# Kernel tuning notes

Measured on AMD Instinct MI355X. Metric: run time of the kernel, lower is better.

The kernel has to match this reference:

```python
import jax, jax.numpy as jnp
import numpy as np
import math

B, S, D = 2, 512, 768
N_HEADS, HEAD = 12, 64
ALPHA = 32.0


def setup_inputs() -> dict:
    key = jax.random.key(0)
    ks = jax.random.split(key, 12)
    w_scale = 1.0 / math.sqrt(D)
    return {
        "hidden_states": jax.random.normal(ks[0], (B, S, D), jnp.float32),
        "attention_mask": jnp.zeros((B, 1, 1, S), jnp.float32),
        "rel_pos": jax.random.normal(ks[1], (B, S, S, HEAD), jnp.float32),
        "rel_2d_pos": jax.random.normal(ks[2], (B, S, S, HEAD), jnp.float32),
        "rel_2d_angle": jax.random.normal(ks[3], (B, S, S, HEAD), jnp.float32),
        "Wq": jax.random.normal(ks[4], (D, D), jnp.float32) * w_scale,
        "bq": jnp.zeros((D,), jnp.float32),
        "Wk": jax.random.normal(ks[5], (D, D), jnp.float32) * w_scale,
        "bk": jnp.zeros((D,), jnp.float32),
        "Wv": jax.random.normal(ks[6], (D, D), jnp.float32) * w_scale,
        "bv": jnp.zeros((D,), jnp.float32),
    }


def _heads(x):
    # (B,S,D) -> (B,N,S,HEAD)
    b, s, _ = x.shape
    return x.reshape(b, s, N_HEADS, HEAD).transpose(0, 2, 1, 3)


def reference(hidden_states, attention_mask, rel_pos, rel_2d_pos, rel_2d_angle,
              Wq, bq, Wk, bk, Wv, bv):
    q = _heads(hidden_states @ Wq.T + bq)
    k = _heads(hidden_states @ Wk.T + bk)
    v = _heads(hidden_states @ Wv.T + bv)

    qs = q / math.sqrt(HEAD)  # scaled query, (B,N,S,HEAD)
    scores = jnp.einsum('bnsh,bnkh->bnsk', qs, k)
    scores = scores + jnp.einsum('bnsh,bskh->bnsk', qs, rel_pos)
    scores = scores + jnp.einsum('bnsh,bskh->bnsk', qs, rel_2d_pos)
    scores = scores + jnp.einsum('bnsh,bskh->bnsk', qs, rel_2d_angle)
    scores = scores + attention_mask

    # cogview (PB-Relax) softmax: subtract per-row max of scores/alpha, rescale
    scaled = scores / ALPHA
    m = jnp.max(scaled, axis=-1, keepdims=True)
    probs = jax.nn.softmax((scaled - m) * ALPHA, axis=-1)

    ctx = jnp.einsum('bnsk,bnkh->bsnh', probs, v)  # (B,S,N,HEAD)
    return ctx.reshape(ctx.shape[0], ctx.shape[1], N_HEADS * HEAD)
```

## Files before the change

### kernel.cpp

```cpp
#include <hip/hip_runtime.h>

typedef __attribute__((ext_vector_type(8))) short short8;
typedef __attribute__((ext_vector_type(4))) float f32x4;

#define B_ 2
#define S_ 512
#define D_ 768
#define NH 12
#define HD 64

__device__ inline short f2bf(float f) {
    union { float f; unsigned u; } v; v.f = f;
    unsigned r = v.u + 0x7fffu + ((v.u >> 16) & 1u);
    return (short)(r >> 16);
}

__device__ __forceinline__ f32x4 ntload4(const float* p) {
    return __builtin_nontemporal_load((const f32x4*)p);
}

__global__ __launch_bounds__(256) void qkv_gemm(
    const float* __restrict__ hidden,
    const float* __restrict__ Wq, const float* __restrict__ Wk, const float* __restrict__ Wv,
    const float* __restrict__ bq, const float* __restrict__ bk, const float* __restrict__ bv,
    short* __restrict__ qbf, short* __restrict__ kbf, short* __restrict__ vbf)
{
    __shared__ short hs[64 * 72];
    __shared__ short wt[64 * 72];

    const int mt = blockIdx.x, nt = blockIdx.y, mat = blockIdx.z;
    const int m0 = mt * 64, n0 = nt * 64;
    const float* W    = (mat == 0) ? Wq : ((mat == 1) ? Wk : Wv);
    const float* bias = (mat == 0) ? bq : ((mat == 1) ? bk : bv);

    const int tid = threadIdx.x;
    const int w = tid >> 6, l = tid & 63;
    const int sr = tid >> 2, sc = (tid & 3) * 16;

    f32x4 acc[4];
    #pragma unroll
    for (int i = 0; i < 4; ++i) acc[i] = (f32x4){0.f, 0.f, 0.f, 0.f};

    const int arow = (w * 16 + (l & 15)) * 72 + (l >> 4) * 8;

    for (int kt = 0; kt < 12; ++kt) {
        const int d0 = kt * 64;
        if (kt) __syncthreads();
        {
            const float4* sa = (const float4*)(hidden + (size_t)(m0 + sr) * D_ + d0 + sc);
            float4 x0 = sa[0], x1 = sa[1], x2 = sa[2], x3 = sa[3];
            short8 p0 = {f2bf(x0.x), f2bf(x0.y), f2bf(x0.z), f2bf(x0.w),
                         f2bf(x1.x), f2bf(x1.y), f2bf(x1.z), f2bf(x1.w)};
            short8 p1 = {f2bf(x2.x), f2bf(x2.y), f2bf(x2.z), f2bf(x2.w),
                         f2bf(x3.x), f2bf(x3.y), f2bf(x3.z), f2bf(x3.w)};
            *(short8*)&hs[sr * 72 + sc]     = p0;
            *(short8*)&hs[sr * 72 + sc + 8] = p1;
            const float4* sb = (const float4*)(W + (size_t)(n0 + sr) * D_ + d0 + sc);
            float4 y0 = sb[0], y1 = sb[1], y2 = sb[2], y3 = sb[3];
            short8 q0 = {f2bf(y0.x), f2bf(y0.y), f2bf(y0.z), f2bf(y0.w),
                         f2bf(y1.x), f2bf(y1.y), f2bf(y1.z), f2bf(y1.w)};
            short8 q1 = {f2bf(y2.x), f2bf(y2.y), f2bf(y2.z), f2bf(y2.w),
                         f2bf(y3.x), f2bf(y3.y), f2bf(y3.z), f2bf(y3.w)};
            *(short8*)&wt[sr * 72 + sc]     = q0;
            *(short8*)&wt[sr * 72 + sc + 8] = q1;
        }
        __syncthreads();
        short8 a0 = *(const short8*)&hs[arow];
        short8 a1 = *(const short8*)&hs[arow + 32];
        #pragma unroll
        for (int ct = 0; ct < 4; ++ct) {
            const int brow = (ct * 16 + (l & 15)) * 72 + (l >> 4) * 8;
            short8 b0 = *(const short8*)&wt[brow];
            short8 b1 = *(const short8*)&wt[brow + 32];
            acc[ct] = __builtin_amdgcn_mfma_f32_16x16x32_bf16(a0, b0, acc[ct], 0, 0, 0);
            acc[ct] = __builtin_amdgcn_mfma_f32_16x16x32_bf16(a1, b1, acc[ct], 0, 0, 0);
        }
    }

    if (mat == 2) {
        __syncthreads();
        #pragma unroll
        for (int ct = 0; ct < 4; ++ct) {
            #pragma unroll
            for (int rr = 0; rr < 4; ++rr) {
                const int m_l = w * 16 + (l >> 4) * 4 + rr;
                const int n_l = ct * 16 + (l & 15);
                hs[n_l * 68 + m_l] = f2bf(acc[ct][rr] + bias[n0 + n_l]);
            }
        }
        __syncthreads();
        const int b   = m0 >> 9;
        const int s0b = m0 & 511;
        #pragma unroll
        for (int j = 0; j < 2; ++j) {
            const int idx  = j * 256 + tid;
            const int h    = idx >> 3;
            const int sseg = (idx & 7) * 8;
            short8 vv = *(const short8*)&hs[h * 68 + sseg];
            *(short8*)(vbf + ((size_t)(b * NH + nt) * HD + h) * S_ + s0b + sseg) = vv;
        }
    } else {
        #pragma unroll
        for (int ct = 0; ct < 4; ++ct) {
            #pragma unroll
            for (int rr = 0; rr < 4; ++rr) {
                const int m_l = w * 16 + (l >> 4) * 4 + rr;
                const int n_l = ct * 16 + (l & 15);
                const int m = m0 + m_l;
                const int b = m >> 9, s = m & 511;
                float v = acc[ct][rr] + bias[n0 + n_l];
                const size_t dst = (((size_t)(b * NH + nt) * S_) + s) * HD + n_l;
                if (mat == 0) qbf[dst] = f2bf(v * 0.125f);
                else          kbf[dst] = f2bf(v);
            }
        }
    }
}

__global__ __launch_bounds__(256) void score_rel(
    const short* __restrict__ qbf,
    const float* __restrict__ rel1, const float* __restrict__ rel2, const float* __restrict__ rel3,
    float* __restrict__ relsc)
{
    const int kt = blockIdx.x;
    const int s  = blockIdx.y;
    const int b  = blockIdx.z;
    const int tid = threadIdx.x;
    const int w = tid >> 6, l = tid & 63;

    const int rowsel = l & 15;
    const int hc     = (l >> 4) * 8;

    const int kc = kt * 4 + w;
    const size_t rbase = ((size_t)(b * S_ + s)) * S_ * HD;
    const size_t ro = rbase + (size_t)(kc * 16 + rowsel) * HD + hc;

    f32x4 p0a = ntload4(rel1 + ro);
    f32x4 p0b = ntload4(rel1 + ro + 4);
    f32x4 q0a = ntload4(rel1 + ro + 32);
    f32x4 q0b = ntload4(rel1 + ro + 36);
    f32x4 p1a = ntload4(rel2 + ro);
    f32x4 p1b = ntload4(rel2 + ro + 4);
    f32x4 q1a = ntload4(rel2 + ro + 32);
    f32x4 q1b = ntload4(rel2 + ro + 36);
    f32x4 p2a = ntload4(rel3 + ro);
    f32x4 p2b = ntload4(rel3 + ro + 4);
    f32x4 q2a = ntload4(rel3 + ro + 32);
    f32x4 q2b = ntload4(rel3 + ro + 36);

    short8 a0 = {0, 0, 0, 0, 0, 0, 0, 0};
    short8 a1 = {0, 0, 0, 0, 0, 0, 0, 0};
    if (rowsel < NH) {
        const short* qp = qbf + (((size_t)(b * NH + rowsel) * S_) + s) * HD;
        a0 = *(const short8*)(qp + hc);
        a1 = *(const short8*)(qp + hc + 32);
    }

    short8 b0 = {
        f2bf(p0a.x + p1a.x + p2a.x), f2bf(p0a.y + p1a.y + p2a.y),
        f2bf(p0a.z + p1a.z + p2a.z), f2bf(p0a.w + p1a.w + p2a.w),
        f2bf(p0b.x + p1b.x + p2b.x), f2bf(p0b.y + p1b.y + p2b.y),
        f2bf(p0b.z + p1b.z + p2b.z), f2bf(p0b.w + p1b.w + p2b.w)};
    short8 b1 = {
        f2bf(q0a.x + q1a.x + q2a.x), f2bf(q0a.y + q1a.y + q2a.y),
        f2bf(q0a.z + q1a.z + q2a.z), f2bf(q0a.w + q1a.w + q2a.w),
        f2bf(q0b.x + q1b.x + q2b.x), f2bf(q0b.y + q1b.y + q2b.y),
        f2bf(q0b.z + q1b.z + q2b.z), f2bf(q0b.w + q1b.w + q2b.w)};

    f32x4 acc = (f32x4){0.f, 0.f, 0.f, 0.f};
    acc = __builtin_amdgcn_mfma_f32_16x16x32_bf16(a0, b0, acc, 0, 0, 0);
    acc = __builtin_amdgcn_mfma_f32_16x16x32_bf16(a1, b1, acc, 0, 0, 0);

    const int kg = kc * 16 + rowsel;
    #pragma unroll
    for (int rr = 0; rr < 4; ++rr) {
        const int n = (l >> 4) * 4 + rr;
        if (n < NH)
            relsc[(((size_t)(b * S_ + s)) * NH + n) * S_ + kg] = acc[rr];
    }
}

__global__ __launch_bounds__(256) void smqkpv(
    const short* __restrict__ qbf, const short* __restrict__ kbf,
    const float* __restrict__ relsc, const float* __restrict__ mask,
    const short* __restrict__ vbf, float* __restrict__ out)
{
    __shared__ float sc[16][520];
    __shared__ short pbf[16][520];

    const int st  = blockIdx.x;
    const int n   = blockIdx.y;
    const int b   = blockIdx.z;
    const int s0  = st * 16;
    const int tid = threadIdx.x;
    const int w = tid >> 6, l = tid & 63;

    const int arow = l & 15;
    const int g    = l >> 4;

    const short* qp = qbf + (((size_t)(b * NH + n) * S_) + s0 + arow) * HD + g * 8;
    short8 a0 = *(const short8*)(qp);
    short8 a1 = *(const short8*)(qp + 32);

    f32x4 acc[8];
    #pragma unroll
    for (int t = 0; t < 8; ++t) acc[t] = (f32x4){0.f, 0.f, 0.f, 0.f};

    #pragma unroll
    for (int t = 0; t < 8; ++t) {
        const int k0 = (w * 8 + t) * 16;
        const short* kp = kbf + (((size_t)(b * NH + n) * S_) + k0 + arow) * HD + g * 8;
        short8 b0 = *(const short8*)(kp);
        short8 b1 = *(const short8*)(kp + 32);
        acc[t] = __builtin_amdgcn_mfma_f32_16x16x32_bf16(a0, b0, acc[t], 0, 0, 0);
        acc[t] = __builtin_amdgcn_mfma_f32_16x16x32_bf16(a1, b1, acc[t], 0, 0, 0);
    }

    #pragma unroll
    for (int t = 0; t < 8; ++t) {
        const int k0 = (w * 8 + t) * 16;
        #pragma unroll
        for (int rr = 0; rr < 4; ++rr)
            sc[g * 4 + rr][k0 + arow] = acc[t][rr];
    }
    __syncthreads();

    #pragma unroll
    for (int j = 0; j < 8; ++j) {
        const int fidx = j * 256 + tid;
        const int row  = fidx >> 7;
        const int c4   = (fidx & 127) * 4;
        float4 r = *(const float4*)(relsc +
                    (((size_t)(b * S_ + s0 + row)) * NH + n) * S_ + c4);
        float4 mk = *(const float4*)(mask + b * S_ + c4);
        float4 cur = *(const float4*)&sc[row][c4];
        cur.x += r.x + mk.x; cur.y += r.y + mk.y;
        cur.z += r.z + mk.z; cur.w += r.w + mk.w;
        *(float4*)&sc[row][c4] = cur;
    }
    __syncthreads();

    const int lane = l;
    for (int r = 0; r < 4; ++r) {
        const int row = w * 4 + r;
        float vals[8];
        float m = -1e30f;
        #pragma unroll
        for (int i = 0; i < 8; ++i) { vals[i] = sc[row][lane + 64 * i]; m = fmaxf(m, vals[i]); }
        #pragma unroll
        for (int off = 32; off >= 1; off >>= 1) m = fmaxf(m, __shfl_xor(m, off));
        float sum = 0.f;
        #pragma unroll
        for (int i = 0; i < 8; ++i) { vals[i] = __expf(vals[i] - m); sum += vals[i]; }
        #pragma unroll
        for (int off = 32; off >= 1; off >>= 1) sum += __shfl_xor(sum, off);
        const float inv = 1.0f / sum;
        #pragma unroll
        for (int i = 0; i < 8; ++i) pbf[row][lane + 64 * i] = f2bf(vals[i] * inv);
    }
    __syncthreads();

    f32x4 pacc = (f32x4){0.f, 0.f, 0.f, 0.f};
    const short* vrow = vbf + ((size_t)(b * NH + n) * HD + w * 16 + arow) * S_ + g * 8;
    #pragma unroll
    for (int kk = 0; kk < 16; ++kk) {
        short8 aP = *(const short8*)&pbf[arow][kk * 32 + g * 8];
        short8 bV = *(const short8*)(vrow + kk * 32);
        pacc = __builtin_amdgcn_mfma_f32_16x16x32_bf16(aP, bV, pacc, 0, 0, 0);
    }
    #pragma unroll
    for (int rr = 0; rr < 4; ++rr) {
        const int srow = g * 4 + rr;
        out[((size_t)(b * S_ + s0 + srow)) * D_ + n * HD + w * 16 + arow] = pacc[rr];
    }
}

extern "C" void kernel_launch(void* const* d_in, const int* in_sizes, int n_in,
                              void* d_out, int out_size, void* d_ws, size_t ws_size,
                              hipStream_t stream) {
    const float* hidden = (const float*)d_in[0];
    const float* mask   = (const float*)d_in[1];
    const float* rel1   = (const float*)d_in[2];
    const float* rel2   = (const float*)d_in[3];
    const float* rel3   = (const float*)d_in[4];
    const float* Wq     = (const float*)d_in[5];
    const float* bq     = (const float*)d_in[6];
    const float* Wk     = (const float*)d_in[7];
    const float* bk     = (const float*)d_in[8];
    const float* Wv     = (const float*)d_in[9];
    const float* bv     = (const float*)d_in[10];
    float* out = (float*)d_out;

    const size_t per = (size_t)B_ * NH * S_ * HD;
    short* qbf   = (short*)d_ws;
    short* kbf   = qbf + per;
    short* vbf   = kbf + per;
    float* relsc = (float*)(vbf + per);

    qkv_gemm<<<dim3(16, 12, 3), 256, 0, stream>>>(hidden, Wq, Wk, Wv, bq, bk, bv, qbf, kbf, vbf);
    score_rel<<<dim3(8, S_, B_), 256, 0, stream>>>(qbf, rel1, rel2, rel3, relsc);
    smqkpv<<<dim3(S_ / 16, NH, B_), 256, 0, stream>>>(qbf, kbf, relsc, mask, vbf, out);
}
```

Measured before the change: 128.9 us.

## Restructure attention: separate QK score kernel, fuse rel-pos scores with softmax and PV

Splits the QK^T+mask into its own tiled MFMA kernel that writes full scores, then fuses the rel-position score computation, softmax and PV into one kernel per (b,s) query row that handles all 12 heads. This removes the relsc round trip, although the qks buffer is the same size. PV now runs as scalar FP32 FMAs that re-read V from global for each query row, instead of using MFMA. That adds a lot of V traffic and ALU work per row in exchange for the fusion.

Measured after the change: 199.6 us. 54.9% more time.

```diff
diff --git a/kernel.cpp b/kernel.cpp
--- a/kernel.cpp
+++ b/kernel.cpp
@@ -13,6 +13,12 @@
     union { float f; unsigned u; } v; v.f = f;
     unsigned r = v.u + 0x7fffu + ((v.u >> 16) & 1u);
     return (short)(r >> 16);
+}
+
+__device__ __forceinline__ float bf2f(short s) {
+    union { unsigned u; float f; } v;
+    v.u = ((unsigned)(unsigned short)s) << 16;
+    return v.f;
 }
 
 __device__ __forceinline__ f32x4 ntload4(const float* p) {
@@ -117,36 +123,73 @@
     }
 }
 
-__global__ __launch_bounds__(256) void score_rel(
+__global__ __launch_bounds__(256) void score_qk(
+    const short* __restrict__ qbf, const short* __restrict__ kbf,
+    const float* __restrict__ mask, float* __restrict__ qks)
+{
+    __shared__ short qa[64 * 72];
+    __shared__ short kb[64 * 72];
+
+    const int st = blockIdx.x, ktile = blockIdx.y, z = blockIdx.z;
+    const int b = z / NH, n = z % NH;
+    const int s0 = st * 64, k0 = ktile * 64;
+    const int tid = threadIdx.x;
+    const int w = tid >> 6, l = tid & 63;
+    const int sr = tid >> 2, sc = (tid & 3) * 16;
+
+    {
+        const short8* sa = (const short8*)(qbf + (((size_t)(b * NH + n) * S_) + s0 + sr) * HD + sc);
+        *(short8*)&qa[sr * 72 + sc]     = sa[0];
+        *(short8*)&qa[sr * 72 + sc + 8] = sa[1];
+        const short8* sb = (const short8*)(kbf + (((size_t)(b * NH + n) * S_) + k0 + sr) * HD + sc);
+        *(short8*)&kb[sr * 72 + sc]     = sb[0];
+        *(short8*)&kb[sr * 72 + sc + 8] = sb[1];
+    }
+    __syncthreads();
+
+    f32x4 acc[4];
+    #pragma unroll
+    for (int i = 0; i < 4; ++i) acc[i] = (f32x4){0.f, 0.f, 0.f, 0.f};
+
+    const int arow = (w * 16 + (l & 15)) * 72 + (l >> 4) * 8;
+    short8 a0 = *(const short8*)&qa[arow];
+    short8 a1 = *(const short8*)&qa[arow + 32];
+    #pragma unroll
+    for (int ct = 0; ct < 4; ++ct) {
+        const int brow = (ct * 16 + (l & 15)) * 72 + (l >> 4) * 8;
+        short8 b0 = *(const short8*)&kb[brow];
+        short8 b1 = *(const short8*)&kb[brow + 32];
+        acc[ct] = __builtin_amdgcn_mfma_f32_16x16x32_bf16(a0, b0, acc[ct], 0, 0, 0);
+        acc[ct] = __builtin_amdgcn_mfma_f32_16x16x32_bf16(a1, b1, acc[ct], 0, 0, 0);
+    }
+
+    #pragma unroll
+    for (int ct = 0; ct < 4; ++ct) {
+        const float mv = mask[b * S_ + k0 + ct * 16 + (l & 15)];
+        #pragma unroll
+        for (int rr = 0; rr < 4; ++rr) {
+            const int s_l = w * 16 + (l >> 4) * 4 + rr;
+            qks[(((size_t)(b * NH + n) * S_) + s0 + s_l) * S_ + k0 + ct * 16 + (l & 15)]
+                = acc[ct][rr] + mv;
+        }
+    }
+}
+
+__global__ __launch_bounds__(256) void fused_rel(
     const short* __restrict__ qbf,
     const float* __restrict__ rel1, const float* __restrict__ rel2, const float* __restrict__ rel3,
-    float* __restrict__ relsc)
+    const float* __restrict__ qks, const short* __restrict__ vbf,
+    float* __restrict__ out)
 {
-    const int kt = blockIdx.x;
-    const int s  = blockIdx.y;
-    const int b  = blockIdx.z;
+    __shared__ float sc[NH][520];
+
+    const int s = blockIdx.x;
+    const int b = blockIdx.y;
     const int tid = threadIdx.x;
     const int w = tid >> 6, l = tid & 63;
 
     const int rowsel = l & 15;
     const int hc     = (l >> 4) * 8;
-
-    const int kc = kt * 4 + w;
-    const size_t rbase = ((size_t)(b * S_ + s)) * S_ * HD;
-    const size_t ro = rbase + (size_t)(kc * 16 + rowsel) * HD + hc;
-
-    f32x4 p0a = ntload4(rel1 + ro);
-    f32x4 p0b = ntload4(rel1 + ro + 4);
-    f32x4 q0a = ntload4(rel1 + ro + 32);
-    f32x4 q0b = ntload4(rel1 + ro + 36);
-    f32x4 p1a = ntload4(rel2 + ro);
-    f32x4 p1b = ntload4(rel2 + ro + 4);
-    f32x4 q1a = ntload4(rel2 + ro + 32);
-    f32x4 q1b = ntload4(rel2 + ro + 36);
-    f32x4 p2a = ntload4(rel3 + ro);
-    f32x4 p2b = ntload4(rel3 + ro + 4);
-    f32x4 q2a = ntload4(rel3 + ro + 32);
-    f32x4 q2b = ntload4(rel3 + ro + 36);
 
     short8 a0 = {0, 0, 0, 0, 0, 0, 0, 0};
     short8 a1 = {0, 0, 0, 0, 0, 0, 0, 0};
@@ -156,97 +199,67 @@
         a1 = *(const short8*)(qp + hc + 32);
     }
 
-    short8 b0 = {
-        f2bf(p0a.x + p1a.x + p2a.x), f2bf(p0a.y + p1a.y + p2a.y),
-        f2bf(p0a.z + p1a.z + p2a.z), f2bf(p0a.w + p1a.w + p2a.w),
-        f2bf(p0b.x + p1b.x + p2b.x), f2bf(p0b.y + p1b.y + p2b.y),
-        f2bf(p0b.z + p1b.z + p2b.z), f2bf(p0b.w + p1b.w + p2b.w)};
-    short8 b1 = {
-        f2bf(q0a.x + q1a.x + q2a.x), f2bf(q0a.y + q1a.y + q2a.y),
-        f2bf(q0a.z + q1a.z + q2a.z), f2bf(q0a.w + q1a.w + q2a.w),
-        f2bf(q0b.x + q1b.x + q2b.x), f2bf(q0b.y + q1b.y + q2b.y),
-        f2bf(q0b.z + q1b.z + q2b.z), f2bf(q0b.w + q1b.w + q2b.w)};
-
-    f32x4 acc = (f32x4){0.f, 0.f, 0.f, 0.f};
-    acc = __builtin_amdgcn_mfma_f32_16x16x32_bf16(a0, b0, acc, 0, 0, 0);
-    acc = __builtin_amdgcn_mfma_f32_16x16x32_bf16(a1, b1, acc, 0, 0, 0);
-
-    const int kg = kc * 16 + rowsel;
-    #pragma unroll
-    for (int rr = 0; rr < 4; ++rr) {
-        const int n = (l >> 4) * 4 + rr;
-        if (n < NH)
-            relsc[(((size_t)(b * S_ + s)) * NH + n) * S_ + kg] = acc[rr];
-    }
-}
-
-__global__ __launch_bounds__(256) void smqkpv(
-    const short* __restrict__ qbf, const short* __restrict__ kbf,
-    const float* __restrict__ relsc, const float* __restrict__ mask,
-    const short* __restrict__ vbf, float* __restrict__ out)
-{
-    __shared__ float sc[16][520];
-    __shared__ short pbf[16][520];
-
-    const int st  = blockIdx.x;
-    const int n   = blockIdx.y;
-    const int b   = blockIdx.z;
-    const int s0  = st * 16;
-    const int tid = threadIdx.x;
-    const int w = tid >> 6, l = tid & 63;
-
-    const int arow = l & 15;
-    const int g    = l >> 4;
-
-    const short* qp = qbf + (((size_t)(b * NH + n) * S_) + s0 + arow) * HD + g * 8;
-    short8 a0 = *(const short8*)(qp);
-    short8 a1 = *(const short8*)(qp + 32);
-
-    f32x4 acc[8];
-    #pragma unroll
-    for (int t = 0; t < 8; ++t) acc[t] = (f32x4){0.f, 0.f, 0.f, 0.f};
-
-    #pragma unroll
+    const size_t rbase = ((size_t)(b * S_ + s)) * S_ * HD;
+
     for (int t = 0; t < 8; ++t) {
-        const int k0 = (w * 8 + t) * 16;
-        const short* kp = kbf + (((size_t)(b * NH + n) * S_) + k0 + arow) * HD + g * 8;
-        short8 b0 = *(const short8*)(kp);
-        short8 b1 = *(const short8*)(kp + 32);
-        acc[t] = __builtin_amdgcn_mfma_f32_16x16x32_bf16(a0, b0, acc[t], 0, 0, 0);
-        acc[t] = __builtin_amdgcn_mfma_f32_16x16x32_bf16(a1, b1, acc[t], 0, 0, 0);
-    }
-
-    #pragma unroll
-    for (int t = 0; t < 8; ++t) {
-        const int k0 = (w * 8 + t) * 16;
-        #pragma unroll
-        for (int rr = 0; rr < 4; ++rr)
-            sc[g * 4 + rr][k0 + arow] = acc[t][rr];
+        const int kc = t * 4 + w;
+        const size_t ro = rbase + (size_t)(kc * 16 + rowsel) * HD + hc;
+
+        f32x4 p0a = ntload4(rel1 + ro);
+        f32x4 p0b = ntload4(rel1 + ro + 4);
+        f32x4 q0a = ntload4(rel1 + ro + 32);
+        f32x4 q0b = ntload4(rel1 + ro + 36);
+        f32x4 p1a = ntload4(rel2 + ro);
+        f32x4 p1b = ntload4(rel2 + ro + 4);
+        f32x4 q1a = ntload4(rel2 + ro + 32);
+        f32x4 q1b = ntload4(rel2 + ro + 36);
+        f32x4 p2a = ntload4(rel3 + ro);
+        f32x4 p2b = ntload4(rel3 + ro + 4);
+        f32x4 q2a = ntload4(rel3 + ro + 32);
+        f32x4 q2b = ntload4(rel3 + ro + 36);
+
+        short8 b0 = {
+            f2bf(p0a.x + p1a.x + p2a.x), f2bf(p0a.y + p1a.y + p2a.y),
+            f2bf(p0a.z + p1a.z + p2a.z), f2bf(p0a.w + p1a.w + p2a.w),
+            f2bf(p0b.x + p1b.x + p2b.x), f2bf(p0b.y + p1b.y + p2b.y),
+            f2bf(p0b.z + p1b.z + p2b.z), f2bf(p0b.w + p1b.w + p2b.w)};
+        short8 b1 = {
+            f2bf(q0a.x + q1a.x + q2a.x), f2bf(q0a.y + q1a.y + q2a.y),
+            f2bf(q0a.z + q1a.z + q2a.z), f2bf(q0a.w + q1a.w + q2a.w),
+            f2bf(q0b.x + q1b.x + q2b.x), f2bf(q0b.y + q1b.y + q2b.y),
+            f2bf(q0b.z + q1b.z + q2b.z), f2bf(q0b.w + q1b.w + q2b.w)};
+
+        f32x4 acc = (f32x4){0.f, 0.f, 0.f, 0.f};
+        acc = __builtin_amdgcn_mfma_f32_16x16x32_bf16(a0, b0, acc, 0, 0, 0);
+        acc = __builtin_amdgcn_mfma_f32_16x16x32_bf16(a1, b1, acc, 0, 0, 0);
+
+        const int kg = kc * 16 + rowsel;
+        #pragma unroll
+        for (int rr = 0; rr < 4; ++rr) {
+            const int n = (l >> 4) * 4 + rr;
+            if (n < NH) sc[n][kg] = acc[rr];
+        }
     }
     __syncthreads();
 
     #pragma unroll
-    for (int j = 0; j < 8; ++j) {
+    for (int j = 0; j < 6; ++j) {
         const int fidx = j * 256 + tid;
         const int row  = fidx >> 7;
         const int c4   = (fidx & 127) * 4;
-        float4 r = *(const float4*)(relsc +
-                    (((size_t)(b * S_ + s0 + row)) * NH + n) * S_ + c4);
-        float4 mk = *(const float4*)(mask + b * S_ + c4);
+        float4 qv = *(const float4*)(qks + (((size_t)(b * NH + row) * S_) + s) * S_ + c4);
         float4 cur = *(const float4*)&sc[row][c4];
-        cur.x += r.x + mk.x; cur.y += r.y + mk.y;
-        cur.z += r.z + mk.z; cur.w += r.w + mk.w;
+        cur.x += qv.x; cur.y += qv.y; cur.z += qv.z; cur.w += qv.w;
         *(float4*)&sc[row][c4] = cur;
     }
     __syncthreads();
 
-    const int lane = l;
-    for (int r = 0; r < 4; ++r) {
-        const int row = w * 4 + r;
+    for (int r = 0; r < 3; ++r) {
+        const int row = r * 4 + w;
         float vals[8];
         float m = -1e30f;
         #pragma unroll
-        for (int i = 0; i < 8; ++i) { vals[i] = sc[row][lane + 64 * i]; m = fmaxf(m, vals[i]); }
+        for (int i = 0; i < 8; ++i) { vals[i] = sc[row][l + 64 * i]; m = fmaxf(m, vals[i]); }
         #pragma unroll
         for (int off = 32; off >= 1; off >>= 1) m = fmaxf(m, __shfl_xor(m, off));
         float sum = 0.f;
@@ -256,23 +269,37 @@
         for (int off = 32; off >= 1; off >>= 1) sum += __shfl_xor(sum, off);
         const float inv = 1.0f / sum;
         #pragma unroll
-        for (int i = 0; i < 8; ++i) pbf[row][lane + 64 * i] = f2bf(vals[i] * inv);
+        for (int i = 0; i < 8; ++i) sc[row][l + 64 * i] = vals[i] * inv;
     }
     __syncthreads();
 
-    f32x4 pacc = (f32x4){0.f, 0.f, 0.f, 0.f};
-    const short* vrow = vbf + ((size_t)(b * NH + n) * HD + w * 16 + arow) * S_ + g * 8;
-    #pragma unroll
-    for (int kk = 0; kk < 16; ++kk) {
-        short8 aP = *(const short8*)&pbf[arow][kk * 32 + g * 8];
-        short8 bV = *(const short8*)(vrow + kk * 32);
-        pacc = __builtin_amdgcn_mfma_f32_16x16x32_bf16(aP, bV, pacc, 0, 0, 0);
-    }
-    #pragma unroll
-    for (int rr = 0; rr < 4; ++rr) {
-        const int srow = g * 4 + rr;
-        out[((size_t)(b * S_ + s0 + srow)) * D_ + n * HD + w * 16 + arow] = pacc[rr];
-    }
+    float res[3];
+    #pragma unroll
+    for (int pi = 0; pi < 3; ++pi) {
+        const int p = pi * 256 + tid;
+        const int n = p >> 6, h = p & 63;
+        const short* vp = vbf + ((size_t)(b * NH + n) * HD + h) * S_;
+        float ax = 0.f, ay = 0.f, az = 0.f, aw = 0.f;
+        #pragma unroll 4
+        for (int k = 0; k < S_; k += 8) {
+            short8 vv = *(const short8*)(vp + k);
+            float4 pa = *(const float4*)&sc[n][k];
+            float4 pb = *(const float4*)&sc[n][k + 4];
+            ax += pa.x * bf2f(vv[0]);
+            ay += pa.y * bf2f(vv[1]);
+            az += pa.z * bf2f(vv[2]);
+            aw += pa.w * bf2f(vv[3]);
+            ax += pb.x * bf2f(vv[4]);
+            ay += pb.y * bf2f(vv[5]);
+            az += pb.z * bf2f(vv[6]);
+            aw += pb.w * bf2f(vv[7]);
+        }
+        res[pi] = (ax + ay) + (az + aw);
+    }
+    float* orow = out + ((size_t)(b * S_ + s)) * D_;
+    #pragma unroll
+    for (int pi = 0; pi < 3; ++pi)
+        orow[pi * 256 + tid] = res[pi];
 }
 
 extern "C" void kernel_launch(void* const* d_in, const int* in_sizes, int n_in,
@@ -292,12 +319,12 @@
     float* out = (float*)d_out;
 
     const size_t per = (size_t)B_ * NH * S_ * HD;
-    short* qbf   = (short*)d_ws;
-    short* kbf   = qbf + per;
-    short* vbf   = kbf + per;
-    float* relsc = (float*)(vbf + per);
+    short* qbf = (short*)d_ws;
+    short* kbf = qbf + per;
+    short* vbf = kbf + per;
+    float* qks = (float*)(vbf + per);
 
     qkv_gemm<<<dim3(16, 12, 3), 256, 0, stream>>>(hidden, Wq, Wk, Wv, bq, bk, bv, qbf, kbf, vbf);
-    score_rel<<<dim3(8, S_, B_), 256, 0, stream>>>(qbf, rel1, rel2, rel3, relsc);
-    smqkpv<<<dim3(S_ / 16, NH, B_), 256, 0, stream>>>(qbf, kbf, relsc, mask, vbf, out);
-}
+    score_qk<<<dim3(8, 8, 24), 256, 0, stream>>>(qbf, kbf, mask, qks);
+    fused_rel<<<dim3(S_, B_), 256, 0, stream>>>(qbf, rel1, rel2, rel3, qks, vbf, out);
+}
```

## Split QK scores into separate tiled kernel, accumulate rel scores in place

Applied to the files above, without the earlier changes.

Moves the QK^T score computation out of the softmax/PV kernel into a new LDS-tiled kernel that writes scores plus mask to the workspace. The relative-position kernel then read-modify-writes its contribution into the same buffer, and the final kernel only runs softmax and PV. This shrinks LDS use in the last kernel and spreads QK across more blocks. In exchange it adds a launch and an extra full read-modify-write pass over the scores buffer.

Result: slower. 134.1 us (+4.0%).

```diff
diff --git a/kernel.cpp b/kernel.cpp
--- a/kernel.cpp
+++ b/kernel.cpp
@@ -117,10 +117,63 @@
     }
 }
 
+__global__ __launch_bounds__(256) void score_qk(
+    const short* __restrict__ qbf, const short* __restrict__ kbf,
+    const float* __restrict__ mask, float* __restrict__ scores)
+{
+    __shared__ short qa[64 * 72];
+    __shared__ short kb[64 * 72];
+
+    const int st = blockIdx.x, ktile = blockIdx.y, z = blockIdx.z;
+    const int b = z / NH, n = z % NH;
+    const int s0 = st * 64, k0 = ktile * 64;
+    const int tid = threadIdx.x;
+    const int w = tid >> 6, l = tid & 63;
+    const int sr = tid >> 2, sc = (tid & 3) * 16;
+
+    {
+        const short8* sa = (const short8*)(qbf + (((size_t)(b * NH + n) * S_) + s0 + sr) * HD + sc);
+        *(short8*)&qa[sr * 72 + sc]     = sa[0];
+        *(short8*)&qa[sr * 72 + sc + 8] = sa[1];
+        const short8* sb = (const short8*)(kbf + (((size_t)(b * NH + n) * S_) + k0 + sr) * HD + sc);
+        *(short8*)&kb[sr * 72 + sc]     = sb[0];
+        *(short8*)&kb[sr * 72 + sc + 8] = sb[1];
+    }
+    __syncthreads();
+
+    f32x4 acc[4];
+    #pragma unroll
+    for (int i = 0; i < 4; ++i) acc[i] = (f32x4){0.f, 0.f, 0.f, 0.f};
+
+    const int arow = (w * 16 + (l & 15)) * 72 + (l >> 4) * 8;
+    short8 a0 = *(const short8*)&qa[arow];
+    short8 a1 = *(const short8*)&qa[arow + 32];
+    #pragma unroll
+    for (int ct = 0; ct < 4; ++ct) {
+        const int brow = (ct * 16 + (l & 15)) * 72 + (l >> 4) * 8;
+        short8 b0 = *(const short8*)&kb[brow];
+        short8 b1 = *(const short8*)&kb[brow + 32];
+        acc[ct] = __builtin_amdgcn_mfma_f32_16x16x32_bf16(a0, b0, acc[ct], 0, 0, 0);
+        acc[ct] = __builtin_amdgcn_mfma_f32_16x16x32_bf16(a1, b1, acc[ct], 0, 0, 0);
+    }
+
+    #pragma unroll
+    for (int ct = 0; ct < 4; ++ct) {
+        const int kcol = k0 + ct * 16 + (l & 15);
+        const float mv = mask[b * S_ + kcol];
+        #pragma unroll
+        for (int rr = 0; rr < 4; ++rr) {
+            const int s_l = w * 16 + (l >> 4) * 4 + rr;
+            scores[(((size_t)(b * S_ + s0 + s_l)) * NH + n) * S_ + kcol]
+                = acc[ct][rr] + mv;
+        }
+    }
+}
+
 __global__ __launch_bounds__(256) void score_rel(
     const short* __restrict__ qbf,
     const float* __restrict__ rel1, const float* __restrict__ rel2, const float* __restrict__ rel3,
-    float* __restrict__ relsc)
+    float* __restrict__ scores)
 {
     const int kt = blockIdx.x;
     const int s  = blockIdx.y;
@@ -175,18 +228,18 @@
     #pragma unroll
     for (int rr = 0; rr < 4; ++rr) {
         const int n = (l >> 4) * 4 + rr;
-        if (n < NH)
-            relsc[(((size_t)(b * S_ + s)) * NH + n) * S_ + kg] = acc[rr];
-    }
-}
-
-__global__ __launch_bounds__(256) void smqkpv(
-    const short* __restrict__ qbf, const short* __restrict__ kbf,
-    const float* __restrict__ relsc, const float* __restrict__ mask,
-    const short* __restrict__ vbf, float* __restrict__ out)
+        if (n < NH) {
+            float* p = scores + (((size_t)(b * S_ + s)) * NH + n) * S_ + kg;
+            *p += acc[rr];
+        }
+    }
+}
+
+__global__ __launch_bounds__(256) void smpv(
+    const float* __restrict__ scores, const short* __restrict__ vbf,
+    float* __restrict__ out)
 {
-    __shared__ float sc[16][520];
-    __shared__ short pbf[16][520];
+    __shared__ short pbf[16][524];
 
     const int st  = blockIdx.x;
     const int n   = blockIdx.y;
@@ -195,71 +248,28 @@
     const int tid = threadIdx.x;
     const int w = tid >> 6, l = tid & 63;
 
+    for (int r = 0; r < 4; ++r) {
+        const int row = w * 4 + r;
+        const float* sp = scores + (((size_t)(b * S_ + s0 + row)) * NH + n) * S_;
+        float vals[8];
+        float m = -1e30f;
+        #pragma unroll
+        for (int i = 0; i < 8; ++i) { vals[i] = sp[l + 64 * i]; m = fmaxf(m, vals[i]); }
+        #pragma unroll
+        for (int off = 32; off >= 1; off >>= 1) m = fmaxf(m, __shfl_xor(m, off));
+        float sum = 0.f;
+        #pragma unroll
+        for (int i = 0; i < 8; ++i) { vals[i] = __expf(vals[i] - m); sum += vals[i]; }
+        #pragma unroll
+        for (int off = 32; off >= 1; off >>= 1) sum += __shfl_xor(sum, off);
+        const float inv = 1.0f / sum;
+        #pragma unroll
+        for (int i = 0; i < 8; ++i) pbf[row][l + 64 * i] = f2bf(vals[i] * inv);
+    }
+    __syncthreads();
+
     const int arow = l & 15;
     const int g    = l >> 4;
-
-    const short* qp = qbf + (((size_t)(b * NH + n) * S_) + s0 + arow) * HD + g * 8;
-    short8 a0 = *(const short8*)(qp);
-    short8 a1 = *(const short8*)(qp + 32);
-
-    f32x4 acc[8];
-    #pragma unroll
-    for (int t = 0; t < 8; ++t) acc[t] = (f32x4){0.f, 0.f, 0.f, 0.f};
-
-    #pragma unroll
-    for (int t = 0; t < 8; ++t) {
-        const int k0 = (w * 8 + t) * 16;
-        const short* kp = kbf + (((size_t)(b * NH + n) * S_) + k0 + arow) * HD + g * 8;
-        short8 b0 = *(const short8*)(kp);
-        short8 b1 = *(const short8*)(kp + 32);
-        acc[t] = __builtin_amdgcn_mfma_f32_16x16x32_bf16(a0, b0, acc[t], 0, 0, 0);
-        acc[t] = __builtin_amdgcn_mfma_f32_16x16x32_bf16(a1, b1, acc[t], 0, 0, 0);
-    }
-
-    #pragma unroll
-    for (int t = 0; t < 8; ++t) {
-        const int k0 = (w * 8 + t) * 16;
-        #pragma unroll
-        for (int rr = 0; rr < 4; ++rr)
-            sc[g * 4 + rr][k0 + arow] = acc[t][rr];
-    }
-    __syncthreads();
-
-    #pragma unroll
-    for (int j = 0; j < 8; ++j) {
-        const int fidx = j * 256 + tid;
-        const int row  = fidx >> 7;
-        const int c4   = (fidx & 127) * 4;
-        float4 r = *(const float4*)(relsc +
-                    (((size_t)(b * S_ + s0 + row)) * NH + n) * S_ + c4);
-        float4 mk = *(const float4*)(mask + b * S_ + c4);
-        float4 cur = *(const float4*)&sc[row][c4];
-        cur.x += r.x + mk.x; cur.y += r.y + mk.y;
-        cur.z += r.z + mk.z; cur.w += r.w + mk.w;
-        *(float4*)&sc[row][c4] = cur;
-    }
-    __syncthreads();
-
-    const int lane = l;
-    for (int r = 0; r < 4; ++r) {
-        const int row = w * 4 + r;
-        float vals[8];
-        float m = -1e30f;
-        #pragma unroll
-        for (int i = 0; i < 8; ++i) { vals[i] = sc[row][lane + 64 * i]; m = fmaxf(m, vals[i]); }
-        #pragma unroll
-        for (int off = 32; off >= 1; off >>= 1) m = fmaxf(m, __shfl_xor(m, off));
-        float sum = 0.f;
-        #pragma unroll
-        for (int i = 0; i < 8; ++i) { vals[i] = __expf(vals[i] - m); sum += vals[i]; }
-        #pragma unroll
-        for (int off = 32; off >= 1; off >>= 1) sum += __shfl_xor(sum, off);
-        const float inv = 1.0f / sum;
-        #pragma unroll
-        for (int i = 0; i < 8; ++i) pbf[row][lane + 64 * i] = f2bf(vals[i] * inv);
-    }
-    __syncthreads();
-
     f32x4 pacc = (f32x4){0.f, 0.f, 0.f, 0.f};
     const short* vrow = vbf + ((size_t)(b * NH + n) * HD + w * 16 + arow) * S_ + g * 8;
     #pragma unroll
@@ -292,12 +302,13 @@
     float* out = (float*)d_out;
 
     const size_t per = (size_t)B_ * NH * S_ * HD;
-    short* qbf   = (short*)d_ws;
-    short* kbf   = qbf + per;
-    short* vbf   = kbf + per;
-    float* relsc = (float*)(vbf + per);
+    short* qbf    = (short*)d_ws;
+    short* kbf    = qbf + per;
+    short* vbf    = kbf + per;
+    float* scores = (float*)(vbf + per);
 
     qkv_gemm<<<dim3(16, 12, 3), 256, 0, stream>>>(hidden, Wq, Wk, Wv, bq, bk, bv, qbf, kbf, vbf);
-    score_rel<<<dim3(8, S_, B_), 256, 0, stream>>>(qbf, rel1, rel2, rel3, relsc);
-    smqkpv<<<dim3(S_ / 16, NH, B_), 256, 0, stream>>>(qbf, kbf, relsc, mask, vbf, out);
-}
+    score_qk<<<dim3(8, 8, 24), 256, 0, stream>>>(qbf, kbf, mask, scores);
+    score_rel<<<dim3(8, S_, B_), 256, 0, stream>>>(qbf, rel1, rel2, rel3, scores);
+    smpv<<<dim3(S_ / 16, NH, B_), 256, 0, stream>>>(scores, vbf, out);
+}
```

## Split Q projection, fuse K/V projection into rel-score kernel, store rel scores as bf16

Applied to the files above, without the earlier changes.

Only the Q projection now runs as its own kernel. The K and V projection blocks are appended to the relative-position score kernel's grid, so they overlap with the bandwidth-bound rel streaming. The rel-score intermediate is stored as bf16 instead of fp32, which halves its write and read traffic. The softmax kernel now adds the rel scores and mask on the fly while loading rows, so the extra shared-memory pass and its barrier are gone. The cost is lower precision for the rel-score term and a heterogeneous grid.

Measured after the change: 130.3 us. Within noise of the previous version (+1.1%).

```diff
diff --git a/kernel.cpp b/kernel.cpp
--- a/kernel.cpp
+++ b/kernel.cpp
@@ -1,4 +1,5 @@
 #include <hip/hip_runtime.h>
+#include <hip/hip_bf16.h>
 
 typedef __attribute__((ext_vector_type(8))) short short8;
 typedef __attribute__((ext_vector_type(4))) float f32x4;
@@ -9,30 +10,28 @@
 #define NH 12
 #define HD 64
 
-__device__ inline short f2bf(float f) {
-    union { float f; unsigned u; } v; v.f = f;
-    unsigned r = v.u + 0x7fffu + ((v.u >> 16) & 1u);
-    return (short)(r >> 16);
+__device__ __forceinline__ short f2bf(float f) {
+    union { __hip_bfloat16 h; short s; } u;
+    u.h = __float2bfloat16(f);
+    return u.s;
+}
+
+__device__ __forceinline__ float bf2f(short s) {
+    union { unsigned u; float f; } v;
+    v.u = ((unsigned)(unsigned short)s) << 16;
+    return v.f;
 }
 
 __device__ __forceinline__ f32x4 ntload4(const float* p) {
     return __builtin_nontemporal_load((const f32x4*)p);
 }
 
-__global__ __launch_bounds__(256) void qkv_gemm(
-    const float* __restrict__ hidden,
-    const float* __restrict__ Wq, const float* __restrict__ Wk, const float* __restrict__ Wv,
-    const float* __restrict__ bq, const float* __restrict__ bk, const float* __restrict__ bv,
-    short* __restrict__ qbf, short* __restrict__ kbf, short* __restrict__ vbf)
+__device__ __forceinline__ void proj_body(
+    const float* __restrict__ hidden, const float* __restrict__ W,
+    const float* __restrict__ bias, int mt, int nt, int mat,
+    short* __restrict__ dst, short* hs, short* wt)
 {
-    __shared__ short hs[64 * 72];
-    __shared__ short wt[64 * 72];
-
-    const int mt = blockIdx.x, nt = blockIdx.y, mat = blockIdx.z;
     const int m0 = mt * 64, n0 = nt * 64;
-    const float* W    = (mat == 0) ? Wq : ((mat == 1) ? Wk : Wv);
-    const float* bias = (mat == 0) ? bq : ((mat == 1) ? bk : bv);
-
     const int tid = threadIdx.x;
     const int w = tid >> 6, l = tid & 63;
     const int sr = tid >> 2, sc = (tid & 3) * 16;
@@ -97,9 +96,10 @@
             const int h    = idx >> 3;
             const int sseg = (idx & 7) * 8;
             short8 vv = *(const short8*)&hs[h * 68 + sseg];
-            *(short8*)(vbf + ((size_t)(b * NH + nt) * HD + h) * S_ + s0b + sseg) = vv;
+            *(short8*)(dst + ((size_t)(b * NH + nt) * HD + h) * S_ + s0b + sseg) = vv;
         }
     } else {
+        const float sca = (mat == 0) ? 0.125f : 1.0f;
         #pragma unroll
         for (int ct = 0; ct < 4; ++ct) {
             #pragma unroll
@@ -108,85 +108,109 @@
                 const int n_l = ct * 16 + (l & 15);
                 const int m = m0 + m_l;
                 const int b = m >> 9, s = m & 511;
-                float v = acc[ct][rr] + bias[n0 + n_l];
-                const size_t dst = (((size_t)(b * NH + nt) * S_) + s) * HD + n_l;
-                if (mat == 0) qbf[dst] = f2bf(v * 0.125f);
-                else          kbf[dst] = f2bf(v);
+                float v = (acc[ct][rr] + bias[n0 + n_l]) * sca;
+                dst[(((size_t)(b * NH + nt) * S_) + s) * HD + n_l] = f2bf(v);
             }
         }
     }
 }
 
-__global__ __launch_bounds__(256) void score_rel(
+__global__ __launch_bounds__(256) void qproj(
+    const float* __restrict__ hidden, const float* __restrict__ Wq,
+    const float* __restrict__ bq, short* __restrict__ qbf)
+{
+    __shared__ short hs[64 * 72];
+    __shared__ short wt[64 * 72];
+    proj_body(hidden, Wq, bq, blockIdx.x, blockIdx.y, 0, qbf, hs, wt);
+}
+
+__global__ __launch_bounds__(256) void relkv(
     const short* __restrict__ qbf,
     const float* __restrict__ rel1, const float* __restrict__ rel2, const float* __restrict__ rel3,
-    float* __restrict__ relsc)
+    const float* __restrict__ hidden,
+    const float* __restrict__ Wk, const float* __restrict__ bk,
+    const float* __restrict__ Wv, const float* __restrict__ bv,
+    short* __restrict__ relsc, short* __restrict__ kbf, short* __restrict__ vbf)
 {
-    const int kt = blockIdx.x;
-    const int s  = blockIdx.y;
-    const int b  = blockIdx.z;
+    __shared__ short hs[64 * 72];
+    __shared__ short wt[64 * 72];
+
+    const int bid = blockIdx.x;
     const int tid = threadIdx.x;
-    const int w = tid >> 6, l = tid & 63;
-
-    const int rowsel = l & 15;
-    const int hc     = (l >> 4) * 8;
-
-    const int kc = kt * 4 + w;
-    const size_t rbase = ((size_t)(b * S_ + s)) * S_ * HD;
-    const size_t ro = rbase + (size_t)(kc * 16 + rowsel) * HD + hc;
-
-    f32x4 p0a = ntload4(rel1 + ro);
-    f32x4 p0b = ntload4(rel1 + ro + 4);
-    f32x4 q0a = ntload4(rel1 + ro + 32);
-    f32x4 q0b = ntload4(rel1 + ro + 36);
-    f32x4 p1a = ntload4(rel2 + ro);
-    f32x4 p1b = ntload4(rel2 + ro + 4);
-    f32x4 q1a = ntload4(rel2 + ro + 32);
-    f32x4 q1b = ntload4(rel2 + ro + 36);
-    f32x4 p2a = ntload4(rel3 + ro);
-    f32x4 p2b = ntload4(rel3 + ro + 4);
-    f32x4 q2a = ntload4(rel3 + ro + 32);
-    f32x4 q2b = ntload4(rel3 + ro + 36);
-
-    short8 a0 = {0, 0, 0, 0, 0, 0, 0, 0};
-    short8 a1 = {0, 0, 0, 0, 0, 0, 0, 0};
-    if (rowsel < NH) {
-        const short* qp = qbf + (((size_t)(b * NH + rowsel) * S_) + s) * HD;
-        a0 = *(const short8*)(qp + hc);
-        a1 = *(const short8*)(qp + hc + 32);
-    }
-
-    short8 b0 = {
-        f2bf(p0a.x + p1a.x + p2a.x), f2bf(p0a.y + p1a.y + p2a.y),
-        f2bf(p0a.z + p1a.z + p2a.z), f2bf(p0a.w + p1a.w + p2a.w),
-        f2bf(p0b.x + p1b.x + p2b.x), f2bf(p0b.y + p1b.y + p2b.y),
-        f2bf(p0b.z + p1b.z + p2b.z), f2bf(p0b.w + p1b.w + p2b.w)};
-    short8 b1 = {
-        f2bf(q0a.x + q1a.x + q2a.x), f2bf(q0a.y + q1a.y + q2a.y),
-        f2bf(q0a.z + q1a.z + q2a.z), f2bf(q0a.w + q1a.w + q2a.w),
-        f2bf(q0b.x + q1b.x + q2b.x), f2bf(q0b.y + q1b.y + q2b.y),
-        f2bf(q0b.z + q1b.z + q2b.z), f2bf(q0b.w + q1b.w + q2b.w)};
-
-    f32x4 acc = (f32x4){0.f, 0.f, 0.f, 0.f};
-    acc = __builtin_amdgcn_mfma_f32_16x16x32_bf16(a0, b0, acc, 0, 0, 0);
-    acc = __builtin_amdgcn_mfma_f32_16x16x32_bf16(a1, b1, acc, 0, 0, 0);
-
-    const int kg = kc * 16 + rowsel;
-    #pragma unroll
-    for (int rr = 0; rr < 4; ++rr) {
-        const int n = (l >> 4) * 4 + rr;
-        if (n < NH)
-            relsc[(((size_t)(b * S_ + s)) * NH + n) * S_ + kg] = acc[rr];
+
+    if (bid < 8192) {
+        const int w = tid >> 6, l = tid & 63;
+        const int kt = bid & 7;
+        const int s  = (bid >> 3) & 511;
+        const int b  = bid >> 12;
+
+        const int rowsel = l & 15;
+        const int hc     = (l >> 4) * 8;
+
+        const int kc = kt * 4 + w;
+        const size_t rbase = ((size_t)(b * S_ + s)) * S_ * HD;
+        const size_t ro = rbase + (size_t)(kc * 16 + rowsel) * HD + hc;
+
+        f32x4 p0a = ntload4(rel1 + ro);
+        f32x4 p0b = ntload4(rel1 + ro + 4);
+        f32x4 q0a = ntload4(rel1 + ro + 32);
+        f32x4 q0b = ntload4(rel1 + ro + 36);
+        f32x4 p1a = ntload4(rel2 + ro);
+        f32x4 p1b = ntload4(rel2 + ro + 4);
+        f32x4 q1a = ntload4(rel2 + ro + 32);
+        f32x4 q1b = ntload4(rel2 + ro + 36);
+        f32x4 p2a = ntload4(rel3 + ro);
+        f32x4 p2b = ntload4(rel3 + ro + 4);
+        f32x4 q2a = ntload4(rel3 + ro + 32);
+        f32x4 q2b = ntload4(rel3 + ro + 36);
+
+        short8 a0 = {0, 0, 0, 0, 0, 0, 0, 0};
+        short8 a1 = {0, 0, 0, 0, 0, 0, 0, 0};
+        if (rowsel < NH) {
+            const short* qp = qbf + (((size_t)(b * NH + rowsel) * S_) + s) * HD;
+            a0 = *(const short8*)(qp + hc);
+            a1 = *(const short8*)(qp + hc + 32);
+        }
+
+        short8 b0 = {
+            f2bf(p0a.x + p1a.x + p2a.x), f2bf(p0a.y + p1a.y + p2a.y),
+            f2bf(p0a.z + p1a.z + p2a.z), f2bf(p0a.w + p1a.w + p2a.w),
+            f2bf(p0b.x + p1b.x + p2b.x), f2bf(p0b.y + p1b.y + p2b.y),
+            f2bf(p0b.z + p1b.z + p2b.z), f2bf(p0b.w + p1b.w + p2b.w)};
+        short8 b1 = {
+            f2bf(q0a.x + q1a.x + q2a.x), f2bf(q0a.y + q1a.y + q2a.y),
+            f2bf(q0a.z + q1a.z + q2a.z), f2bf(q0a.w + q1a.w + q2a.w),
+            f2bf(q0b.x + q1b.x + q2b.x), f2bf(q0b.y + q1b.y + q2b.y),
+            f2bf(q0b.z + q1b.z + q2b.z), f2bf(q0b.w + q1b.w + q2b.w)};
+
+        f32x4 acc = (f32x4){0.f, 0.f, 0.f, 0.f};
+        acc = __builtin_amdgcn_mfma_f32_16x16x32_bf16(a0, b0, acc, 0, 0, 0);
+        acc = __builtin_amdgcn_mfma_f32_16x16x32_bf16(a1, b1, acc, 0, 0, 0);
+
+        const int kg = kc * 16 + rowsel;
+        #pragma unroll
+        for (int rr = 0; rr < 4; ++rr) {
+            const int n = (l >> 4) * 4 + rr;
+            if (n < NH)
+                relsc[(((size_t)(b * S_ + s)) * NH + n) * S_ + kg] = f2bf(acc[rr]);
+        }
+    } else {
+        const int j    = bid - 8192;
+        const int mt   = j & 15;
+        const int rest = j >> 4;
+        const int nt   = rest % 12;
+        if (rest < 12) proj_body(hidden, Wk, bk, mt, nt, 1, kbf, hs, wt);
+        else           proj_body(hidden, Wv, bv, mt, nt, 2, vbf, hs, wt);
     }
 }
 
 __global__ __launch_bounds__(256) void smqkpv(
     const short* __restrict__ qbf, const short* __restrict__ kbf,
-    const float* __restrict__ relsc, const float* __restrict__ mask,
+    const short* __restrict__ relsc, const float* __restrict__ mask,
     const short* __restrict__ vbf, float* __restrict__ out)
 {
     __shared__ float sc[16][520];
-    __shared__ short pbf[16][520];
+    __shared__ short pbf[16][524];
 
     const int st  = blockIdx.x;
     const int n   = blockIdx.y;
@@ -225,28 +249,16 @@
     }
     __syncthreads();
 
-    #pragma unroll
-    for (int j = 0; j < 8; ++j) {
-        const int fidx = j * 256 + tid;
-        const int row  = fidx >> 7;
-        const int c4   = (fidx & 127) * 4;
-        float4 r = *(const float4*)(relsc +
-                    (((size_t)(b * S_ + s0 + row)) * NH + n) * S_ + c4);
-        float4 mk = *(const float4*)(mask + b * S_ + c4);
-        float4 cur = *(const float4*)&sc[row][c4];
-        cur.x += r.x + mk.x; cur.y += r.y + mk.y;
-        cur.z += r.z + mk.z; cur.w += r.w + mk.w;
-        *(float4*)&sc[row][c4] = cur;
-    }
-    __syncthreads();
-
-    const int lane = l;
     for (int r = 0; r < 4; ++r) {
         const int row = w * 4 + r;
+        const short* rp = relsc + (((size_t)(b * S_ + s0 + row)) * NH + n) * S_;
         float vals[8];
         float m = -1e30f;
         #pragma unroll
-        for (int i = 0; i < 8; ++i) { vals[i] = sc[row][lane + 64 * i]; m = fmaxf(m, vals[i]); }
+        for (int i = 0; i < 8; ++i) {
+            vals[i] = sc[row][l + 64 * i] + bf2f(rp[l + 64 * i]) + mask[b * S_ + l + 64 * i];
+            m = fmaxf(m, vals[i]);
+        }
         #pragma unroll
         for (int off = 32; off >= 1; off >>= 1) m = fmaxf(m, __shfl_xor(m, off));
         float sum = 0.f;
@@ -256,7 +268,7 @@
         for (int off = 32; off >= 1; off >>= 1) sum += __shfl_xor(sum, off);
         const float inv = 1.0f / sum;
         #pragma unroll
-        for (int i = 0; i < 8; ++i) pbf[row][lane + 64 * i] = f2bf(vals[i] * inv);
+        for (int i = 0; i < 8; ++i) pbf[row][l + 64 * i] = f2bf(vals[i] * inv);
     }
     __syncthreads();
 
@@ -295,9 +307,11 @@
     short* qbf   = (short*)d_ws;
     short* kbf   = qbf + per;
     short* vbf   = kbf + per;
-    float* relsc = (float*)(vbf + per);
-
-    qkv_gemm<<<dim3(16, 12, 3), 256, 0, stream>>>(hidden, Wq, Wk, Wv, bq, bk, bv, qbf, kbf, vbf);
-    score_rel<<<dim3(8, S_, B_), 256, 0, stream>>>(qbf, rel1, rel2, rel3, relsc);
+    short* relsc = vbf + per;
+
+    qproj<<<dim3(16, 12), 256, 0, stream>>>(hidden, Wq, bq, qbf);
+    relkv<<<dim3(8192 + 384), 256, 0, stream>>>(qbf, rel1, rel2, rel3,
+                                                hidden, Wk, bk, Wv, bv,
+                                                relsc, kbf, vbf);
     smqkpv<<<dim3(S_ / 16, NH, B_), 256, 0, stream>>>(qbf, kbf, relsc, mask, vbf, out);
 }
```
